# Kernel optimization log

Measured on AMD Instinct MI355X. Metric: run time of the kernel, lower is better.

Reference implementation:

```python
import jax, jax.numpy as jnp
import numpy as np
import math

B, CIN, COUT, K, H, W, STYLE_DIM = 16, 32, 32, 3, 256, 256, 512


def setup_inputs() -> dict:
    key = jax.random.key(0)
    k1, k2, k3, k4 = jax.random.split(key, 4)
    return {
        "input": jax.random.normal(k1, (B, CIN, H, W), dtype=jnp.float32),
        "style": jax.random.normal(k2, (B, STYLE_DIM), dtype=jnp.float32),
        "weight": jax.random.normal(k3, (1, COUT, CIN, K, K), dtype=jnp.float32),
        "mod_weight": jax.random.normal(k4, (CIN, STYLE_DIM), dtype=jnp.float32),
        "mod_bias": jnp.ones((CIN,), dtype=jnp.float32),  # bias_init=1
    }


def reference(input, style, weight, mod_weight, mod_bias):
    b, cin, h, w = input.shape
    cout = weight.shape[1]
    k = weight.shape[-1]
    eps = 1e-8

    # EqualLinear modulation: scale = 1/sqrt(style_dim), lr_mul = 1
    mscale = 1.0 / math.sqrt(style.shape[1])
    s = style @ (mod_weight * mscale).T + mod_bias            # (B, Cin)

    # scale buffer = 1/sqrt(fan_in), fan_in = cin*k*k (mask is all ones)
    wscale = 1.0 / math.sqrt(cin * k * k)

    # per-sample modulated weights: (B, Cout, Cin, K, K)
    wmod = wscale * weight * s[:, None, :, None, None]
    wmod = wmod.reshape(b * cout, cin, k, k)

    # groups = batch conv, padding = k // 2 (same padding)
    x = input.reshape(1, b * cin, h, w)
    pad = k // 2
    out = jax.lax.conv_general_dilated(
        x, wmod,
        window_strides=(1, 1),
        padding=[(pad, pad), (pad, pad)],
        feature_group_count=b,
        dimension_numbers=("NCHW", "OIHW", "NCHW"),
    )
    out = out.reshape(b, cout, h, w)

    # demod_obj == 'data': divide by per-(b,c) unbiased spatial std
    std = jnp.std(out, axis=(2, 3), keepdims=True, ddof=1)
    return out / std
```

## Files before the change

kernel.cpp:

```cpp
#include <hip/hip_runtime.h>
#include <math.h>

#define CIN   32
#define COUT  32
#define HH    256
#define WW    256
#define BB    16
#define SDIM  512

#define XT    16
#define YT    16
#define NXT   16
#define NTILE 256

typedef __attribute__((ext_vector_type(8))) short bf16x8;
typedef __attribute__((ext_vector_type(4))) float f32x4;
typedef __attribute__((ext_vector_type(8))) unsigned short u16x8;

__device__ __forceinline__ unsigned bf16_rne_bits(float x) {
    unsigned u = __float_as_uint(x);
    return (u + 0x7fffu + ((u >> 16) & 1u)) >> 16;
}

__global__ __launch_bounds__(256) void fused_prep_kernel(
    const float* __restrict__ input,
    const float* __restrict__ style,
    const float* __restrict__ mod_weight,
    const float* __restrict__ mod_bias,
    const float* __restrict__ weight,
    unsigned short* __restrict__ nhwc,
    unsigned short* __restrict__ Wk,
    float* __restrict__ zbuf) {
    __shared__ __align__(16) unsigned short lt[256 * 40];
    const int bid = blockIdx.x;
    const int tid = threadIdx.x;

    if (bid < 4096) {
        const int gy = bid & 255;
        const int b  = bid >> 8;

        #pragma unroll
        for (int it = 0; it < 2; ++it) {
            int idx = it * 256 + tid;
            int xf  = idx & 63;
            int cg  = idx >> 6;
            const float* ip = input + (((b * 32 + cg * 4) * 256 + gy) * 256) + xf * 4;
            float4 v0 = *(const float4*)(ip);
            float4 v1 = *(const float4*)(ip + 65536);
            float4 v2 = *(const float4*)(ip + 131072);
            float4 v3 = *(const float4*)(ip + 196608);
            float a0[4] = {v0.x, v0.y, v0.z, v0.w};
            float a1[4] = {v1.x, v1.y, v1.z, v1.w};
            float a2[4] = {v2.x, v2.y, v2.z, v2.w};
            float a3[4] = {v3.x, v3.y, v3.z, v3.w};
            #pragma unroll
            for (int m = 0; m < 4; ++m) {
                uint2 p;
                p.x = bf16_rne_bits(a0[m]) | (bf16_rne_bits(a1[m]) << 16);
                p.y = bf16_rne_bits(a2[m]) | (bf16_rne_bits(a3[m]) << 16);
                *(uint2*)&lt[(xf * 4 + m) * 40 + cg * 4] = p;
            }
        }
        __syncthreads();

        unsigned short* cb = nhwc + (((((b << 8) + gy) << 8)) << 5);
        #pragma unroll
        for (int it = 0; it < 4; ++it) {
            int idx  = it * 256 + tid;
            int slot = idx & 3;
            int gx   = idx >> 2;
            int o    = (slot - ((gx + 1) >> 1)) & 3;
            bf16x8 v = *(const bf16x8*)&lt[gx * 40 + o * 8];
            *(bf16x8*)(cb + (gx << 5) + slot * 8) = v;
        }
    } else {
        const int wblk = bid - 4096;
        const int b    = wblk / 36;
        if (wblk == 0 && tid < 16) zbuf[tid] = 0.f;

        float* s_lds = (float*)lt;
        if (tid < 32) {
            const int ci = tid;
            const float mscale = 0.044194173824159216f;
            const float* st = style + b * SDIM;
            const float* mw = mod_weight + ci * SDIM;
            float acc = 0.f;
            for (int d = 0; d < SDIM; d += 4) {
                acc += st[d]   * mw[d]
                     + st[d+1] * mw[d+1]
                     + st[d+2] * mw[d+2]
                     + st[d+3] * mw[d+3];
            }
            s_lds[ci] = acc * mscale + mod_bias[ci];
        }
        __syncthreads();

        const int idx = wblk * 256 + tid;
        const float wscale = 0.05892556509887896f;
        int r  = idx % (COUT * CIN * 9);
        int co = r / (CIN * 9);
        int r2 = r % (CIN * 9);
        int ci = r2 / 9;
        int w  = r2 % 9;
        float wm = wscale * weight[co * (CIN * 9) + ci * 9 + w] * s_lds[ci];
        unsigned hb = bf16_rne_bits(wm);
        float hif = __uint_as_float(hb << 16);
        unsigned lb = bf16_rne_bits(wm - hif);
        int base = ((b * 9 + w) * 2) * 1024 + co * 32 + ci;
        Wk[base]        = (unsigned short)hb;
        Wk[base + 1024] = (unsigned short)lb;
    }
}

__global__ __launch_bounds__(256, 6) void conv_mfma_kernel(
    const unsigned short* __restrict__ nhwc,
    const unsigned short* __restrict__ Wk,
    const float* __restrict__ zbuf,
    unsigned short* __restrict__ bfout,
    float2* __restrict__ partials) {

    __shared__ __align__(16) unsigned short xlds[18 * 576];
    __shared__ float2 stats[4 * 32];

    const int tid = threadIdx.x;
    const int wg = blockIdx.x;
    const int sw = (wg & 7) * 512 + (wg >> 3);
    const int b  = sw >> 8;
    const int yt = (sw >> 4) & 15;
    const int xt = sw & 15;

    const int x0 = xt * XT, y0 = yt * YT;
    const int t  = tid & 15;
    const int g  = (tid >> 4) & 3;
    const int wv = tid >> 6;
    const int f  = wv & 1;
    const int rbase = 8 * (wv >> 1);

    #pragma unroll
    for (int it = 0; it < 6; ++it) {
        int idx = it * 256 + tid;
        if (idx < 1296) {
            int s  = idx & 3;
            int cu = idx >> 2;
            int u  = cu % 18;
            int y  = cu / 18;
            int gy = y0 - 1 + y, gx = x0 - 1 + u;
            bool ok = ((unsigned)gy < 256u) && ((unsigned)gx < 256u);
            const unsigned short* src = ok
                ? nhwc + (((((b << 8) + gy) << 8) + gx) << 5) + s * 8
                : (const unsigned short*)zbuf + s * 8;
            __builtin_amdgcn_global_load_lds(
                (const __attribute__((address_space(1))) unsigned int*)src,
                (__attribute__((address_space(3))) unsigned int*)
                    ((char*)xlds + (idx << 4)),
                16, 0, 0);
        }
    }
    __syncthreads();

    f32x4 acc[8];
    #pragma unroll
    for (int i = 0; i < 8; ++i) acc[i] = (f32x4){0.f, 0.f, 0.f, 0.f};

    #pragma unroll 1
    for (int kw = 0; kw < 3; ++kw) {
        const int u = t + kw;
        const int slot = (g + (u >> 1)) & 3;

        bf16x8 wf[3];
        const unsigned short* wb =
            Wk + (b * 9 * 2) * 1024 + f * 512 + t * 32 + g * 8;
        #pragma unroll
        for (int kh = 0; kh < 3; ++kh)
            wf[kh] = *(const bf16x8*)(wb + ((kh * 3 + kw) * 2) * 1024);

        bf16x8 xv[10];
        #pragma unroll
        for (int y = 0; y < 10; ++y)
            xv[y] = *(const bf16x8*)&xlds[(rbase + y) * 576 + u * 32 + slot * 8];

        #pragma unroll
        for (int kh = 0; kh < 3; ++kh)
            #pragma unroll
            for (int i = 0; i < 8; ++i)
                acc[i] = __builtin_amdgcn_mfma_f32_16x16x32_bf16(
                    wf[kh], xv[i + kh], acc[i], 0, 0, 0);
    }

    float s_[4] = {0.f, 0.f, 0.f, 0.f}, q_[4] = {0.f, 0.f, 0.f, 0.f};
    #pragma unroll
    for (int i = 0; i < 8; ++i) {
        const int gy = y0 + rbase + i;
        #pragma unroll
        for (int r = 0; r < 4; ++r) {
            float v = acc[i][r];
            const int off = (b * 32 + 16 * f + 4 * g + r) * 65536 + gy * 256 + x0 + t;
            bfout[off] = (unsigned short)bf16_rne_bits(v);
            s_[r] += v;
            q_[r] += v * v;
        }
    }
    #pragma unroll
    for (int r = 0; r < 4; ++r) {
        #pragma unroll
        for (int off = 1; off < 16; off <<= 1) {
            s_[r] += __shfl_xor(s_[r], off);
            q_[r] += __shfl_xor(q_[r], off);
        }
    }
    if (t == 0) {
        #pragma unroll
        for (int r = 0; r < 4; ++r)
            stats[wv * 32 + 16 * f + 4 * g + r] = make_float2(s_[r], q_[r]);
    }
    __syncthreads();
    if (tid < 32) {
        int w0 = (tid < 16) ? 0 : 1;
        float2 a = stats[w0 * 32 + tid];
        float2 c = stats[(w0 + 2) * 32 + tid];
        partials[(b * 32 + tid) * NTILE + yt * NXT + xt] =
            make_float2(a.x + c.x, a.y + c.y);
    }
}

__global__ __launch_bounds__(256) void reduce_scale_kernel(
    const float2* __restrict__ partials,
    const unsigned short* __restrict__ bf,
    float* __restrict__ out) {
    __shared__ float wsum[4], wsq[4];
    __shared__ float inv_s;
    const int bid = blockIdx.x;
    const int c   = bid >> 2;
    const int q   = bid & 3;
    const int tid = threadIdx.x;

    float2 p = partials[c * 256 + tid];
    float s = p.x, sq = p.y;
    #pragma unroll
    for (int off = 1; off < 64; off <<= 1) {
        s  += __shfl_xor(s,  off);
        sq += __shfl_xor(sq, off);
    }
    if ((tid & 63) == 0) { wsum[tid >> 6] = s; wsq[tid >> 6] = sq; }
    __syncthreads();
    if (tid == 0) {
        float S = wsum[0] + wsum[1] + wsum[2] + wsum[3];
        float Q = wsq[0]  + wsq[1]  + wsq[2]  + wsq[3];
        const float N = 65536.f;
        float var = (Q - S * S / N) / (N - 1.f);
        inv_s = 1.0f / sqrtf(var);
    }
    __syncthreads();
    const float m = inv_s;

    const unsigned short* src = bf  + c * 65536 + q * 16384;
    float*                dst = out + c * 65536 + q * 16384;
    #pragma unroll
    for (int it = 0; it < 8; ++it) {
        int i = (it * 256 + tid) * 8;
        u16x8 v = *(const u16x8*)&src[i];
        float4 a, cc;
        a.x  = __uint_as_float(((unsigned)v[0]) << 16) * m;
        a.y  = __uint_as_float(((unsigned)v[1]) << 16) * m;
        a.z  = __uint_as_float(((unsigned)v[2]) << 16) * m;
        a.w  = __uint_as_float(((unsigned)v[3]) << 16) * m;
        cc.x = __uint_as_float(((unsigned)v[4]) << 16) * m;
        cc.y = __uint_as_float(((unsigned)v[5]) << 16) * m;
        cc.z = __uint_as_float(((unsigned)v[6]) << 16) * m;
        cc.w = __uint_as_float(((unsigned)v[7]) << 16) * m;
        *(float4*)&dst[i]     = a;
        *(float4*)&dst[i + 4] = cc;
    }
}

extern "C" void kernel_launch(void* const* d_in, const int* in_sizes, int n_in,
                              void* d_out, int out_size, void* d_ws, size_t ws_size,
                              hipStream_t stream) {
    const float* input      = (const float*)d_in[0];
    const float* style      = (const float*)d_in[1];
    const float* weight     = (const float*)d_in[2];
    const float* mod_weight = (const float*)d_in[3];
    const float* mod_bias   = (const float*)d_in[4];
    float* out = (float*)d_out;
    char*  ws  = (char*)d_ws;

    unsigned short* Wk       = (unsigned short*)(ws + 2048);
    float2*         partials = (float2*)(ws + 2048 + 589824);
    float*          zbuf     = (float*)(ws + 2048 + 589824 + 1048576 + 2048);
    const size_t    bf_off   = 2048 + 589824 + 1048576 + 2048 + 64;
    unsigned short* bfout    = (unsigned short*)(ws + bf_off);

    unsigned short* nhwc = (unsigned short*)d_out;

    fused_prep_kernel<<<4672, 256, 0, stream>>>(
        input, style, mod_weight, mod_bias, weight, nhwc, Wk, zbuf);
    conv_mfma_kernel<<<4096, 256, 0, stream>>>(nhwc, Wk, zbuf, bfout, partials);
    reduce_scale_kernel<<<2048, 256, 0, stream>>>(partials, bfout, out);
}
```

Before: 113.2 us.

## Load conv input fragments directly from global memory instead of LDS staging

Removes the LDS halo tile and its async global-to-LDS fill plus barrier in the conv kernel. Each wave now loads its bf16x8 input fragments straight from the NHWC global buffer, pointing out-of-bounds rows and columns at a zero buffer. The launch-bounds occupancy hint is also dropped. This cuts LDS use and the sync point, but each input element is now reloaded from global memory/cache by multiple waves and kw iterations, raising global traffic and load latency per MFMA.

```diff
diff --git a/kernel.cpp b/kernel.cpp
--- a/kernel.cpp
+++ b/kernel.cpp
@@ -112,14 +112,13 @@
     }
 }
 
-__global__ __launch_bounds__(256, 6) void conv_mfma_kernel(
+__global__ __launch_bounds__(256) void conv_mfma_kernel(
     const unsigned short* __restrict__ nhwc,
     const unsigned short* __restrict__ Wk,
-    const float* __restrict__ zbuf,
+    const unsigned short* __restrict__ zbuf16,
     unsigned short* __restrict__ bfout,
     float2* __restrict__ partials) {
 
-    __shared__ __align__(16) unsigned short xlds[18 * 576];
     __shared__ float2 stats[4 * 32];
 
     const int tid = threadIdx.x;
@@ -136,35 +135,15 @@
     const int f  = wv & 1;
     const int rbase = 8 * (wv >> 1);
 
-    #pragma unroll
-    for (int it = 0; it < 6; ++it) {
-        int idx = it * 256 + tid;
-        if (idx < 1296) {
-            int s  = idx & 3;
-            int cu = idx >> 2;
-            int u  = cu % 18;
-            int y  = cu / 18;
-            int gy = y0 - 1 + y, gx = x0 - 1 + u;
-            bool ok = ((unsigned)gy < 256u) && ((unsigned)gx < 256u);
-            const unsigned short* src = ok
-                ? nhwc + (((((b << 8) + gy) << 8) + gx) << 5) + s * 8
-                : (const unsigned short*)zbuf + s * 8;
-            __builtin_amdgcn_global_load_lds(
-                (const __attribute__((address_space(1))) unsigned int*)src,
-                (__attribute__((address_space(3))) unsigned int*)
-                    ((char*)xlds + (idx << 4)),
-                16, 0, 0);
-        }
-    }
-    __syncthreads();
-
     f32x4 acc[8];
     #pragma unroll
     for (int i = 0; i < 8; ++i) acc[i] = (f32x4){0.f, 0.f, 0.f, 0.f};
 
     #pragma unroll 1
     for (int kw = 0; kw < 3; ++kw) {
-        const int u = t + kw;
+        const int u  = t + kw;
+        const int gx = x0 - 1 + u;
+        const bool col_ok = (unsigned)gx < 256u;
         const int slot = (g + (u >> 1)) & 3;
 
         bf16x8 wf[3];
@@ -175,9 +154,16 @@
             wf[kh] = *(const bf16x8*)(wb + ((kh * 3 + kw) * 2) * 1024);
 
         bf16x8 xv[10];
-        #pragma unroll
-        for (int y = 0; y < 10; ++y)
-            xv[y] = *(const bf16x8*)&xlds[(rbase + y) * 576 + u * 32 + slot * 8];
+        const unsigned short* colbase =
+            nhwc + ((((b << 8) << 8) + gx) << 5) + slot * 8;
+        const unsigned short* zp = zbuf16 + slot * 8;
+        #pragma unroll
+        for (int y = 0; y < 10; ++y) {
+            const int gy = y0 - 1 + rbase + y;
+            const bool ok = col_ok && ((unsigned)gy < 256u);
+            const unsigned short* p = ok ? colbase + ((long)gy << 13) : zp;
+            xv[y] = *(const bf16x8*)p;
+        }
 
         #pragma unroll
         for (int kh = 0; kh < 3; ++kh)
@@ -294,6 +280,7 @@
 
     fused_prep_kernel<<<4672, 256, 0, stream>>>(
         input, style, mod_weight, mod_bias, weight, nhwc, Wk, zbuf);
-    conv_mfma_kernel<<<4096, 256, 0, stream>>>(nhwc, Wk, zbuf, bfout, partials);
+    conv_mfma_kernel<<<4096, 256, 0, stream>>>(
+        nhwc, Wk, (const unsigned short*)zbuf, bfout, partials);
     reduce_scale_kernel<<<2048, 256, 0, stream>>>(partials, bfout, out);
 }
```

Result: slower. 121.5 us (+7.3%).

## Shrink conv workgroup to two waves looping over two 8-row sub-tiles

Applied to the files above, without the earlier changes.

The conv kernel now uses 128 threads (two waves, one per output-channel half) instead of four waves. Each workgroup processes its 16x16 tile as two sequential 8-row sub-tiles, reloading a 10-row halo into a smaller LDS buffer each time. This cuts LDS per block and the cross-wave stats reduction, which may allow more resident blocks. In exchange it adds redundant halo-row loads, an extra barrier per sub-tile, and serializes load and compute within each block.

```diff
diff --git a/kernel.cpp b/kernel.cpp
--- a/kernel.cpp
+++ b/kernel.cpp
@@ -9,7 +9,6 @@
 #define SDIM  512
 
 #define XT    16
-#define YT    16
 #define NXT   16
 #define NTILE 256
 
@@ -112,94 +111,101 @@
     }
 }
 
-__global__ __launch_bounds__(256, 6) void conv_mfma_kernel(
+__global__ __launch_bounds__(128) void conv_mfma_kernel(
     const unsigned short* __restrict__ nhwc,
     const unsigned short* __restrict__ Wk,
     const float* __restrict__ zbuf,
     unsigned short* __restrict__ bfout,
     float2* __restrict__ partials) {
 
-    __shared__ __align__(16) unsigned short xlds[18 * 576];
-    __shared__ float2 stats[4 * 32];
+    __shared__ __align__(16) unsigned short xlds[10 * 576];
+    __shared__ float2 stats[32];
 
     const int tid = threadIdx.x;
-    const int wg = blockIdx.x;
-    const int sw = (wg & 7) * 512 + (wg >> 3);
-    const int b  = sw >> 8;
-    const int yt = (sw >> 4) & 15;
-    const int xt = sw & 15;
-
-    const int x0 = xt * XT, y0 = yt * YT;
+    const int wg  = blockIdx.x;
+    const int sw  = (wg & 7) * 512 + (wg >> 3);
+    const int b   = sw >> 8;
+    const int ytp = (sw >> 4) & 15;
+    const int xt  = sw & 15;
+
+    const int x0 = xt * XT;
     const int t  = tid & 15;
     const int g  = (tid >> 4) & 3;
-    const int wv = tid >> 6;
-    const int f  = wv & 1;
-    const int rbase = 8 * (wv >> 1);
-
-    #pragma unroll
-    for (int it = 0; it < 6; ++it) {
-        int idx = it * 256 + tid;
-        if (idx < 1296) {
-            int s  = idx & 3;
-            int cu = idx >> 2;
-            int u  = cu % 18;
-            int y  = cu / 18;
-            int gy = y0 - 1 + y, gx = x0 - 1 + u;
-            bool ok = ((unsigned)gy < 256u) && ((unsigned)gx < 256u);
-            const unsigned short* src = ok
-                ? nhwc + (((((b << 8) + gy) << 8) + gx) << 5) + s * 8
-                : (const unsigned short*)zbuf + s * 8;
-            __builtin_amdgcn_global_load_lds(
-                (const __attribute__((address_space(1))) unsigned int*)src,
-                (__attribute__((address_space(3))) unsigned int*)
-                    ((char*)xlds + (idx << 4)),
-                16, 0, 0);
-        }
-    }
-    __syncthreads();
-
-    f32x4 acc[8];
-    #pragma unroll
-    for (int i = 0; i < 8; ++i) acc[i] = (f32x4){0.f, 0.f, 0.f, 0.f};
+    const int f  = tid >> 6;
+
+    float s_[4] = {0.f, 0.f, 0.f, 0.f}, q_[4] = {0.f, 0.f, 0.f, 0.f};
 
     #pragma unroll 1
-    for (int kw = 0; kw < 3; ++kw) {
-        const int u = t + kw;
-        const int slot = (g + (u >> 1)) & 3;
-
-        bf16x8 wf[3];
-        const unsigned short* wb =
-            Wk + (b * 9 * 2) * 1024 + f * 512 + t * 32 + g * 8;
-        #pragma unroll
-        for (int kh = 0; kh < 3; ++kh)
-            wf[kh] = *(const bf16x8*)(wb + ((kh * 3 + kw) * 2) * 1024);
-
-        bf16x8 xv[10];
-        #pragma unroll
-        for (int y = 0; y < 10; ++y)
-            xv[y] = *(const bf16x8*)&xlds[(rbase + y) * 576 + u * 32 + slot * 8];
-
-        #pragma unroll
-        for (int kh = 0; kh < 3; ++kh)
-            #pragma unroll
-            for (int i = 0; i < 8; ++i)
-                acc[i] = __builtin_amdgcn_mfma_f32_16x16x32_bf16(
-                    wf[kh], xv[i + kh], acc[i], 0, 0, 0);
-    }
-
-    float s_[4] = {0.f, 0.f, 0.f, 0.f}, q_[4] = {0.f, 0.f, 0.f, 0.f};
-    #pragma unroll
-    for (int i = 0; i < 8; ++i) {
-        const int gy = y0 + rbase + i;
-        #pragma unroll
-        for (int r = 0; r < 4; ++r) {
-            float v = acc[i][r];
-            const int off = (b * 32 + 16 * f + 4 * g + r) * 65536 + gy * 256 + x0 + t;
-            bfout[off] = (unsigned short)bf16_rne_bits(v);
-            s_[r] += v;
-            q_[r] += v * v;
-        }
-    }
+    for (int sub = 0; sub < 2; ++sub) {
+        const int y0 = ytp * 16 + sub * 8;
+
+        #pragma unroll
+        for (int it = 0; it < 6; ++it) {
+            int idx = it * 128 + tid;
+            if (idx < 720) {
+                int s  = idx & 3;
+                int cu = idx >> 2;
+                int u  = cu % 18;
+                int y  = cu / 18;
+                int gy = y0 - 1 + y, gx = x0 - 1 + u;
+                bool ok = ((unsigned)gy < 256u) && ((unsigned)gx < 256u);
+                const unsigned short* src = ok
+                    ? nhwc + (((((b << 8) + gy) << 8) + gx) << 5) + s * 8
+                    : (const unsigned short*)zbuf + s * 8;
+                __builtin_amdgcn_global_load_lds(
+                    (const __attribute__((address_space(1))) unsigned int*)src,
+                    (__attribute__((address_space(3))) unsigned int*)
+                        ((char*)xlds + (idx << 4)),
+                    16, 0, 0);
+            }
+        }
+        __syncthreads();
+
+        f32x4 acc[8];
+        #pragma unroll
+        for (int i = 0; i < 8; ++i) acc[i] = (f32x4){0.f, 0.f, 0.f, 0.f};
+
+        #pragma unroll 1
+        for (int kw = 0; kw < 3; ++kw) {
+            const int u = t + kw;
+            const int slot = (g + (u >> 1)) & 3;
+
+            bf16x8 wf[3];
+            const unsigned short* wb =
+                Wk + (b * 9 * 2) * 1024 + f * 512 + t * 32 + g * 8;
+            #pragma unroll
+            for (int kh = 0; kh < 3; ++kh)
+                wf[kh] = *(const bf16x8*)(wb + ((kh * 3 + kw) * 2) * 1024);
+
+            bf16x8 xv[10];
+            #pragma unroll
+            for (int y = 0; y < 10; ++y)
+                xv[y] = *(const bf16x8*)&xlds[y * 576 + u * 32 + slot * 8];
+
+            #pragma unroll
+            for (int kh = 0; kh < 3; ++kh)
+                #pragma unroll
+                for (int i = 0; i < 8; ++i)
+                    acc[i] = __builtin_amdgcn_mfma_f32_16x16x32_bf16(
+                        wf[kh], xv[i + kh], acc[i], 0, 0, 0);
+        }
+
+        #pragma unroll
+        for (int i = 0; i < 8; ++i) {
+            const int gy = y0 + i;
+            #pragma unroll
+            for (int r = 0; r < 4; ++r) {
+                float v = acc[i][r];
+                const int off =
+                    (b * 32 + 16 * f + 4 * g + r) * 65536 + gy * 256 + x0 + t;
+                bfout[off] = (unsigned short)bf16_rne_bits(v);
+                s_[r] += v;
+                q_[r] += v * v;
+            }
+        }
+        __syncthreads();
+    }
+
     #pragma unroll
     for (int r = 0; r < 4; ++r) {
         #pragma unroll
@@ -211,16 +217,11 @@
     if (t == 0) {
         #pragma unroll
         for (int r = 0; r < 4; ++r)
-            stats[wv * 32 + 16 * f + 4 * g + r] = make_float2(s_[r], q_[r]);
+            stats[16 * f + 4 * g + r] = make_float2(s_[r], q_[r]);
     }
     __syncthreads();
-    if (tid < 32) {
-        int w0 = (tid < 16) ? 0 : 1;
-        float2 a = stats[w0 * 32 + tid];
-        float2 c = stats[(w0 + 2) * 32 + tid];
-        partials[(b * 32 + tid) * NTILE + yt * NXT + xt] =
-            make_float2(a.x + c.x, a.y + c.y);
-    }
+    if (tid < 32)
+        partials[(b * 32 + tid) * NTILE + ytp * NXT + xt] = stats[tid];
 }
 
 __global__ __launch_bounds__(256) void reduce_scale_kernel(
@@ -294,6 +295,6 @@
 
     fused_prep_kernel<<<4672, 256, 0, stream>>>(
         input, style, mod_weight, mod_bias, weight, nhwc, Wk, zbuf);
-    conv_mfma_kernel<<<4096, 256, 0, stream>>>(nhwc, Wk, zbuf, bfout, partials);
+    conv_mfma_kernel<<<4096, 128, 0, stream>>>(nhwc, Wk, zbuf, bfout, partials);
     reduce_scale_kernel<<<2048, 256, 0, stream>>>(partials, bfout, out);
 }
```

Result: slower. 117.6 us (+3.9%).
